# Kernel tuning notes

Hardware: AMD Instinct MI355X
Metric: run time of the kernel (lower is better)

## Reference

```python
import jax, jax.numpy as jnp
import numpy as np

IN_FEATURES = 4096
OUT_FEATURES = 11008
BLOCK_SIZE = 64
BITS = 4
RANGE_MAX = 2 ** (BITS - 1) - 1  # 7


def setup_inputs() -> dict:
    key = jax.random.key(0)
    k1, k2, k3, k4 = jax.random.split(key, 4)
    n_blocks = OUT_FEATURES * IN_FEATURES // BLOCK_SIZE
    x = jax.random.normal(k1, (4, 2048, IN_FEATURES), dtype=jnp.float32)
    # int4 codes in [-7, 7]; stored signed int. Use randint in [-7, 8).
    weight_quant = jax.random.randint(k2, (n_blocks, BLOCK_SIZE), -RANGE_MAX, RANGE_MAX + 1, dtype=jnp.int32)
    weight_absmax = jax.random.uniform(k3, (n_blocks, 1), dtype=jnp.float32, minval=1e-5, maxval=1.0)
    bias = jax.random.normal(k4, (OUT_FEATURES,), dtype=jnp.float32)
    return {"x": x, "weight_quant": weight_quant, "weight_absmax": weight_absmax, "bias": bias}


def reference(x, weight_quant, weight_absmax, bias):
    # Blockwise dequant: q/range_max * absmax per block, reshape to (out, in). padding=0.
    w = (weight_quant.astype(jnp.float32) / RANGE_MAX) * weight_absmax  # [n_blocks, block]
    w = w.reshape(OUT_FEATURES, IN_FEATURES)
    # F.linear: y = x @ W^T + b
    return jnp.einsum('bsi,oi->bso', x, w) + bias
```

## Files before the change

### kernel.cpp

```cpp
#include <hip/hip_runtime.h>


#define K_DIM 4096
#define N_DIM 11008
#define M_DIM 8192
#define NT_K 64

typedef _Float16 f16;
typedef _Float16 f16x8 __attribute__((ext_vector_type(8)));
typedef float f32x4 __attribute__((ext_vector_type(4)));

__device__ __forceinline__ void gload16(const void* g, void* lds) {
  __builtin_amdgcn_global_load_lds(
      (__attribute__((address_space(1))) void*)g,
      (__attribute__((address_space(3))) void*)lds,
      16, 0, 0);
}

__global__ __launch_bounds__(256) void cvt_x_kernel(const float* __restrict__ x,
                                                    f16* __restrict__ xo, int n8) {
  int i = blockIdx.x * blockDim.x + threadIdx.x;
  if (i >= n8) return;
  const float4* xv = (const float4*)x;
  float4 a = xv[2 * i];
  float4 b = xv[2 * i + 1];
  f16x8 o;
  o[0] = (f16)a.x; o[1] = (f16)a.y; o[2] = (f16)a.z; o[3] = (f16)a.w;
  o[4] = (f16)b.x; o[5] = (f16)b.y; o[6] = (f16)b.z; o[7] = (f16)b.w;
  *(f16x8*)(xo + (size_t)i * 8) = o;
}

__global__ __launch_bounds__(256) void dequant_kernel(const int* __restrict__ q,
                                                      const float* __restrict__ amax,
                                                      f16* __restrict__ wo, int n8) {
  int i = blockIdx.x * blockDim.x + threadIdx.x;
  if (i >= n8) return;
  const int4* qv = (const int4*)q;
  int4 a = qv[2 * i];
  int4 b = qv[2 * i + 1];
  float s = amax[i >> 3] * (1.0f / 7.0f);
  f16x8 o;
  o[0] = (f16)((float)a.x * s); o[1] = (f16)((float)a.y * s);
  o[2] = (f16)((float)a.z * s); o[3] = (f16)((float)a.w * s);
  o[4] = (f16)((float)b.x * s); o[5] = (f16)((float)b.y * s);
  o[6] = (f16)((float)b.z * s); o[7] = (f16)((float)b.w * s);
  *(f16x8*)(wo + (size_t)i * 8) = o;
}

__global__ __launch_bounds__(512, 2) void gemm_f16_bt(const f16* __restrict__ A,
                                                      const f16* __restrict__ B,
                                                      const float* __restrict__ bias,
                                                      float* __restrict__ C) {
  __shared__ __align__(16) char lds[131072];

  const int tid = threadIdx.x;
  const int w = tid >> 6;
  const int l = tid & 63;
  const int wr = w >> 2;
  const int wc = w & 3;

  const int wg = blockIdx.x;
  const int swz = (wg & 7) * 172 + (wg >> 3);
  const int mt = swz / 43;
  const int nt = swz % 43;
  const int m0 = mt * 256;
  const int n0 = nt * 256;

  const int lr = l & 15;
  const int g = l >> 4;
  const int laneoff = ((lr >> 1) << 7) | (((((lr & 1) << 6) | (g << 4))) ^ (((lr >> 1) & 7) << 4));

  const char* Asrc[2];
  const char* Bsrc[2];
#pragma unroll
  for (int j = 0; j < 2; ++j) {
    const int u = ((j * 8 + w) << 10) + l * 16;
    const int r = u >> 7;
    const int cp = (u & 127) ^ ((r & 7) << 4);
    const int ra = 2 * r + (cp >> 6);
    const int kb = cp & 63;
    Asrc[j] = (const char*)A + (size_t)(m0 + ra) * (K_DIM * 2) + kb;
    Bsrc[j] = (const char*)B + (size_t)(n0 + ra) * (K_DIM * 2) + kb;
  }

  char* ldsc = (char*)lds;

  f32x4 acc[8][4];
#pragma unroll
  for (int i = 0; i < 8; ++i)
#pragma unroll
    for (int j = 0; j < 4; ++j) acc[i][j] = (f32x4){0.f, 0.f, 0.f, 0.f};

#pragma unroll
  for (int h = 0; h < 2; ++h) {
    const int koff = h * 64;
    char* dA = ldsc + h * 16384 + w * 1024;
    gload16(Asrc[0] + koff, dA);
    gload16(Asrc[1] + koff, dA + 8192);
    char* dB = ldsc + 65536 + h * 16384 + w * 1024;
    gload16(Bsrc[0] + koff, dB);
    gload16(Bsrc[1] + koff, dB + 8192);
  }
  asm volatile("s_waitcnt vmcnt(4)" ::: "memory");
  __builtin_amdgcn_s_barrier();

  for (int t = 0; t < NT_K; ++t) {
    const int p = t & 1;
    const int pn = p ^ 1;
    const int tn = (t + 1 < NT_K) ? (t + 1) : (NT_K - 1);
    const int kA = tn * 128;
    const int Ab = p * 32768;
    const int Bb = 65536 + p * 32768;
    const int An = pn * 32768;
    const int Bn = 65536 + pn * 32768;

    f16x8 bf[4];
    f16x8 af[4];
#pragma unroll
    for (int kk = 0; kk < 2; ++kk) {
#pragma unroll
      for (int mh = 0; mh < 2; ++mh) {
        if (mh == 0) {
#pragma unroll
          for (int ni = 0; ni < 4; ++ni)
            bf[ni] = *(const f16x8*)(ldsc + Bb + kk * 16384 + ((wc * 64 + ni * 16) << 6) + laneoff);
        }
#pragma unroll
        for (int mi = 0; mi < 4; ++mi)
          af[mi] = *(const f16x8*)(ldsc + Ab + kk * 16384 +
                                   ((wr * 128 + mh * 64 + mi * 16) << 6) + laneoff);

        const int pi = kk * 2 + mh;
        if (pi == 0) {
          char* d = ldsc + An + w * 1024;
          gload16(Asrc[0] + kA, d); gload16(Asrc[1] + kA, d + 8192);
        } else if (pi == 1) {
          char* d = ldsc + Bn + w * 1024;
          gload16(Bsrc[0] + kA, d); gload16(Bsrc[1] + kA, d + 8192);
        } else if (pi == 2) {
          char* d = ldsc + An + 16384 + w * 1024;
          gload16(Asrc[0] + kA + 64, d); gload16(Asrc[1] + kA + 64, d + 8192);
        } else {
          char* d = ldsc + Bn + 16384 + w * 1024;
          gload16(Bsrc[0] + kA + 64, d); gload16(Bsrc[1] + kA + 64, d + 8192);
        }

        __builtin_amdgcn_s_barrier();
        __builtin_amdgcn_s_setprio(1);
#pragma unroll
        for (int mi = 0; mi < 4; ++mi)
#pragma unroll
          for (int ni = 0; ni < 4; ++ni)
            acc[mh * 4 + mi][ni] = __builtin_amdgcn_mfma_f32_16x16x32_f16(
                af[mi], bf[ni], acc[mh * 4 + mi][ni], 0, 0, 0);
        __builtin_amdgcn_s_setprio(0);
        if (pi == 1) asm volatile("s_waitcnt vmcnt(4)" ::: "memory");
        if (pi == 3) asm volatile("s_waitcnt vmcnt(4)" ::: "memory");
        __builtin_amdgcn_s_barrier();
      }
    }
  }

  const int orow = g * 4;
  float bv[4];
#pragma unroll
  for (int ni = 0; ni < 4; ++ni) bv[ni] = bias[n0 + wc * 64 + ni * 16 + lr];
#pragma unroll
  for (int mi = 0; mi < 8; ++mi) {
    const int row = m0 + wr * 128 + mi * 16 + orow;
#pragma unroll
    for (int ni = 0; ni < 4; ++ni) {
      const size_t cb = (size_t)row * N_DIM + (n0 + wc * 64 + ni * 16 + lr);
#pragma unroll
      for (int j = 0; j < 4; ++j) C[cb + (size_t)j * N_DIM] = acc[mi][ni][j] + bv[ni];
    }
  }
}

extern "C" void kernel_launch(void* const* d_in, const int* in_sizes, int n_in,
                              void* d_out, int out_size, void* d_ws, size_t ws_size,
                              hipStream_t stream) {
  const float* x = (const float*)d_in[0];
  const int* wq = (const int*)d_in[1];
  const float* amax = (const float*)d_in[2];
  const float* bias = (const float*)d_in[3];
  float* out = (float*)d_out;

  f16* Xh = (f16*)d_ws;
  f16* Wh = (f16*)((char*)d_ws + (size_t)M_DIM * K_DIM * 2);

  {
    int n8 = M_DIM * K_DIM / 8;
    cvt_x_kernel<<<n8 / 256, 256, 0, stream>>>(x, Xh, n8);
  }
  {
    int n8 = N_DIM * K_DIM / 8;
    dequant_kernel<<<n8 / 256, 256, 0, stream>>>(wq, amax, Wh, n8);
  }
  {
    dim3 grid((M_DIM / 256) * (N_DIM / 256));
    gemm_f16_bt<<<grid, 512, 0, stream>>>(Xh, Wh, bias, out);
  }
}
```

Before: 816.0 us.

## Deepen GEMM prefetch pipeline to issue global-to-LDS loads further ahead

Restructures the main GEMM loop's global-to-LDS staging so quarter-tiles are issued up to two K-steps ahead rather than one. Each half-slot of LDS is refilled as soon as the MFMAs that consume it are done, and more loads stay in flight (vmcnt 10 instead of 4). The aim is to hide more global memory latency behind MFMA work within the same 128KB LDS budget. It relies on careful buffer reuse ordering, so a mistake in the slot timing would race with reads still in use.

```diff
diff --git a/kernel.cpp b/kernel.cpp
--- a/kernel.cpp
+++ b/kernel.cpp
@@ -85,79 +85,83 @@
 
   char* ldsc = (char*)lds;
 
+#define STAGE_A(dst_off, koff)                              \
+  {                                                         \
+    char* d_ = ldsc + (dst_off) + w * 1024;                 \
+    gload16(Asrc[0] + (koff), d_);                          \
+    gload16(Asrc[1] + (koff), d_ + 8192);                   \
+  }
+#define STAGE_B(dst_off, koff)                              \
+  {                                                         \
+    char* d_ = ldsc + (dst_off) + w * 1024;                 \
+    gload16(Bsrc[0] + (koff), d_);                          \
+    gload16(Bsrc[1] + (koff), d_ + 8192);                   \
+  }
+
   f32x4 acc[8][4];
 #pragma unroll
   for (int i = 0; i < 8; ++i)
 #pragma unroll
     for (int j = 0; j < 4; ++j) acc[i][j] = (f32x4){0.f, 0.f, 0.f, 0.f};
 
-#pragma unroll
-  for (int h = 0; h < 2; ++h) {
-    const int koff = h * 64;
-    char* dA = ldsc + h * 16384 + w * 1024;
-    gload16(Asrc[0] + koff, dA);
-    gload16(Asrc[1] + koff, dA + 8192);
-    char* dB = ldsc + 65536 + h * 16384 + w * 1024;
-    gload16(Bsrc[0] + koff, dB);
-    gload16(Bsrc[1] + koff, dB + 8192);
-  }
-  asm volatile("s_waitcnt vmcnt(4)" ::: "memory");
+  STAGE_B(65536, 0);
+  STAGE_A(0, 0);
+  STAGE_B(65536 + 16384, 64);
+  STAGE_A(16384, 64);
+  STAGE_B(65536 + 32768, 128);
+  STAGE_A(32768, 128);
+  STAGE_B(65536 + 32768 + 16384, 192);
+  asm volatile("s_waitcnt vmcnt(10)" ::: "memory");
   __builtin_amdgcn_s_barrier();
 
   for (int t = 0; t < NT_K; ++t) {
     const int p = t & 1;
     const int pn = p ^ 1;
-    const int tn = (t + 1 < NT_K) ? (t + 1) : (NT_K - 1);
-    const int kA = tn * 128;
     const int Ab = p * 32768;
     const int Bb = 65536 + p * 32768;
-    const int An = pn * 32768;
-    const int Bn = 65536 + pn * 32768;
+    const int t1 = (t + 1 < NT_K) ? (t + 1) : (NT_K - 1);
+    const int t2 = (t + 2 < NT_K) ? (t + 2) : (NT_K - 1);
+    const int k1 = t1 * 128;
+    const int k2 = t2 * 128;
 
     f16x8 bf[4];
     f16x8 af[4];
 #pragma unroll
-    for (int kk = 0; kk < 2; ++kk) {
-#pragma unroll
-      for (int mh = 0; mh < 2; ++mh) {
-        if (mh == 0) {
-#pragma unroll
-          for (int ni = 0; ni < 4; ++ni)
-            bf[ni] = *(const f16x8*)(ldsc + Bb + kk * 16384 + ((wc * 64 + ni * 16) << 6) + laneoff);
-        }
-#pragma unroll
-        for (int mi = 0; mi < 4; ++mi)
-          af[mi] = *(const f16x8*)(ldsc + Ab + kk * 16384 +
-                                   ((wr * 128 + mh * 64 + mi * 16) << 6) + laneoff);
-
-        const int pi = kk * 2 + mh;
-        if (pi == 0) {
-          char* d = ldsc + An + w * 1024;
-          gload16(Asrc[0] + kA, d); gload16(Asrc[1] + kA, d + 8192);
-        } else if (pi == 1) {
-          char* d = ldsc + Bn + w * 1024;
-          gload16(Bsrc[0] + kA, d); gload16(Bsrc[1] + kA, d + 8192);
-        } else if (pi == 2) {
-          char* d = ldsc + An + 16384 + w * 1024;
-          gload16(Asrc[0] + kA + 64, d); gload16(Asrc[1] + kA + 64, d + 8192);
-        } else {
-          char* d = ldsc + Bn + 16384 + w * 1024;
-          gload16(Bsrc[0] + kA + 64, d); gload16(Bsrc[1] + kA + 64, d + 8192);
-        }
-
-        __builtin_amdgcn_s_barrier();
-        __builtin_amdgcn_s_setprio(1);
-#pragma unroll
-        for (int mi = 0; mi < 4; ++mi)
-#pragma unroll
-          for (int ni = 0; ni < 4; ++ni)
-            acc[mh * 4 + mi][ni] = __builtin_amdgcn_mfma_f32_16x16x32_f16(
-                af[mi], bf[ni], acc[mh * 4 + mi][ni], 0, 0, 0);
-        __builtin_amdgcn_s_setprio(0);
-        if (pi == 1) asm volatile("s_waitcnt vmcnt(4)" ::: "memory");
-        if (pi == 3) asm volatile("s_waitcnt vmcnt(4)" ::: "memory");
-        __builtin_amdgcn_s_barrier();
+    for (int pi = 0; pi < 4; ++pi) {
+      const int kk = pi >> 1;
+      const int mh = pi & 1;
+
+      if (mh == 0) {
+#pragma unroll
+        for (int ni = 0; ni < 4; ++ni)
+          bf[ni] = *(const f16x8*)(ldsc + Bb + kk * 16384 + ((wc * 64 + ni * 16) << 6) + laneoff);
       }
+#pragma unroll
+      for (int mi = 0; mi < 4; ++mi)
+        af[mi] = *(const f16x8*)(ldsc + Ab + kk * 16384 +
+                                 ((wr * 128 + mh * 64 + mi * 16) << 6) + laneoff);
+
+      if (pi == 0) {
+        STAGE_A(pn * 32768 + 16384, k1 + 64);
+      } else if (pi == 1) {
+        STAGE_B(65536 + p * 32768, k2);
+      } else if (pi == 2) {
+        STAGE_A(p * 32768, k2);
+      } else {
+        STAGE_B(65536 + p * 32768 + 16384, k2 + 64);
+      }
+
+      __builtin_amdgcn_s_barrier();
+      __builtin_amdgcn_s_setprio(1);
+#pragma unroll
+      for (int mi = 0; mi < 4; ++mi)
+#pragma unroll
+        for (int ni = 0; ni < 4; ++ni)
+          acc[mh * 4 + mi][ni] = __builtin_amdgcn_mfma_f32_16x16x32_f16(
+              af[mi], bf[ni], acc[mh * 4 + mi][ni], 0, 0, 0);
+      __builtin_amdgcn_s_setprio(0);
+      if (mh == 1) asm volatile("s_waitcnt vmcnt(10)" ::: "memory");
+      __builtin_amdgcn_s_barrier();
     }
   }
 
@@ -175,6 +179,8 @@
       for (int j = 0; j < 4; ++j) C[cb + (size_t)j * N_DIM] = acc[mi][ni][j] + bv[ni];
     }
   }
+#undef STAGE_A
+#undef STAGE_B
 }
 
 extern "C" void kernel_launch(void* const* d_in, const int* in_sizes, int n_in,
```

Result: no change. 820.1 us (+0.5%).
